# Kernel tuning notes

Hardware: AMD Instinct MI355X
Metric: run time of the kernel (lower is better)

The kernel has to match this reference:

```python
import jax, jax.numpy as jnp
import numpy as np

NX, NY, NT = 128, 128, 64          # global space-time grid
LX, LY = 2.0, 2.0                  # periodic domain extents
K_NB = 128                         # neighbors per query
NHEAD = 4
EPS = 1e-5


def setup_inputs() -> dict:
    key = jax.random.key(0)
    ks = jax.random.split(key, 12)
    N = NX * NY * NT
    B, d, dff, L = 2048, 64, 128, 2
    nrm = lambda k, s: jax.random.normal(k, s, jnp.float32) * 0.05
    return {
        "q_lin_idx": jax.random.randint(ks[0], (B,), 0, N),
        "offsets_ijk": jax.random.randint(ks[1], (K_NB, 3), 0, 8),
        "coords": jax.random.uniform(ks[2], (N, 3), jnp.float32) * 2.0,
        "vals": jax.random.normal(ks[3], (N, 3), jnp.float32),
        "log_gammas": jnp.zeros((3,), jnp.float32),
        "proj_w": nrm(ks[4], (d, 6)), "proj_b": jnp.zeros((d,), jnp.float32),
        "qkv_w": nrm(ks[5], (L, 3 * d, d)), "qkv_b": jnp.zeros((L, 3 * d), jnp.float32),
        "out_w": nrm(ks[6], (L, d, d)), "out_b": jnp.zeros((L, d), jnp.float32),
        "ln1_s": jnp.ones((L, d), jnp.float32), "ln1_b": jnp.zeros((L, d), jnp.float32),
        "ff1_w": nrm(ks[7], (L, dff, d)), "ff1_b": jnp.zeros((L, dff), jnp.float32),
        "ff2_w": nrm(ks[8], (L, d, dff)), "ff2_b": jnp.zeros((L, d), jnp.float32),
        "ln2_s": jnp.ones((L, d), jnp.float32), "ln2_b": jnp.zeros((L, d), jnp.float32),
        "head_ln_s": jnp.ones((d,), jnp.float32), "head_ln_b": jnp.zeros((d,), jnp.float32),
        "head1_w": nrm(ks[9], (d, d)), "head1_b": jnp.zeros((d,), jnp.float32),
        "head2_w": nrm(ks[10], (3, d)), "head2_b": jnp.zeros((3,), jnp.float32),
    }


def _ln(x, s, b):
    m = x.mean(-1, keepdims=True)
    v = ((x - m) ** 2).mean(-1, keepdims=True)
    return (x - m) * jax.lax.rsqrt(v + EPS) * s + b


def _dper(a, b, L):
    # periodic relative delta in [-L/2, L/2)
    return (a - b + 0.5 * L) % L - 0.5 * L


def reference(q_lin_idx, offsets_ijk, coords, vals, log_gammas, proj_w, proj_b,
              qkv_w, qkv_b, out_w, out_b, ln1_s, ln1_b, ff1_w, ff1_b, ff2_w, ff2_b,
              ln2_s, ln2_b, head_ln_s, head_ln_b, head1_w, head1_b, head2_w, head2_b):
    # --- periodic-wrapped neighbor indices (div/mod on linear index) ---
    i = q_lin_idx // (NY * NT)
    r = q_lin_idx % (NY * NT)
    j = r // NT
    kk = r % NT
    di, dj, dk = offsets_ijk[:, 0], offsets_ijk[:, 1], offsets_ijk[:, 2]
    I = (i[:, None] + di[None, :]) % NX          # wrap_x
    J = (j[:, None] + dj[None, :]) % NY          # wrap_y
    T = jnp.clip(kk[:, None] + dk[None, :], 0, NT - 1)  # no wrap in t
    nb = I * (NY * NT) + J * NT + T              # [B, K]

    # --- gather + relative-delta encode ---
    q_xyz = coords[q_lin_idx]                    # [B, 3]
    nb_xyz = coords[nb]                          # [B, K, 3]
    dx = _dper(nb_xyz[..., 0], q_xyz[:, None, 0], LX)
    dy = _dper(nb_xyz[..., 1], q_xyz[:, None, 1], LY)
    dt = nb_xyz[..., 2] - q_xyz[:, None, 2]
    rel = jnp.stack([dx, dy, dt], -1) * jnp.exp(log_gammas)[None, None, :]
    tokens = jnp.concatenate([rel, vals[nb]], -1)  # [B, K, 6]

    # --- input projection + TransformerEncoder (post-norm, relu FF) ---
    h = tokens @ proj_w.T + proj_b               # [B, S, d]
    B, S, d = h.shape
    dh = d // NHEAD
    scale = 1.0 / np.sqrt(dh).astype(np.float32)
    for l in range(qkv_w.shape[0]):
        qkv = h @ qkv_w[l].T + qkv_b[l]
        qh, kh, vh = jnp.split(qkv, 3, axis=-1)
        qh = qh.reshape(B, S, NHEAD, dh).transpose(0, 2, 1, 3)
        kh = kh.reshape(B, S, NHEAD, dh).transpose(0, 2, 1, 3)
        vh = vh.reshape(B, S, NHEAD, dh).transpose(0, 2, 1, 3)
        att = jax.nn.softmax(jnp.einsum('bhqd,bhkd->bhqk', qh, kh) * scale, axis=-1)
        o = jnp.einsum('bhqk,bhkd->bhqd', att, vh).transpose(0, 2, 1, 3).reshape(B, S, d)
        h = _ln(h + (o @ out_w[l].T + out_b[l]), ln1_s[l], ln1_b[l])
        ff = jax.nn.relu(h @ ff1_w[l].T + ff1_b[l]) @ ff2_w[l].T + ff2_b[l]
        h = _ln(h + ff, ln2_s[l], ln2_b[l])

    # --- mean pool over neighbors + head ---
    hm = h.mean(axis=1)                          # [B, d]
    g = _ln(hm, head_ln_s, head_ln_b)
    g = jax.nn.gelu(g @ head1_w.T + head1_b, approximate=False)
    return g @ head2_w.T + head2_b               # [B, 3]
```

## Files before the change

### kernel.cpp

```cpp
#include <hip/hip_runtime.h>
#include <math.h>

#define NXg 128
#define NYg 128
#define NTg 64
#define SEQ 128
#define DIM 64
#define NH 4
#define DHd 16
#define DFFd 128
#define NLAYER 2
#define EPSf 1e-5f

typedef _Float16 f16x8 __attribute__((ext_vector_type(8)));
typedef _Float16 f16x4 __attribute__((ext_vector_type(4)));
typedef __fp16 fp16x2 __attribute__((ext_vector_type(2)));
typedef float f32x4 __attribute__((ext_vector_type(4)));

#define MFMA16(a, b, c) __builtin_amdgcn_mfma_f32_16x16x32_f16(a, b, c, 0, 0, 0)

union FragU { int d[4]; f16x8 v; };
union H4U  { int d[2]; f16x4 v; };
union P2U  { int i; fp16x2 h; };

__device__ __forceinline__ int pk2(float a, float b) {
  P2U u;
  u.h = __builtin_amdgcn_cvt_pkrtz(a, b);
  return u.i;
}
__device__ __forceinline__ float2 up2(int p) {
  P2U u; u.i = p;
  return make_float2((float)u.h[0], (float)u.h[1]);
}

__device__ __forceinline__ f16x8 zero8() {
  f16x8 z;
#pragma unroll
  for (int i = 0; i < 8; ++i) z[i] = (_Float16)0.0f;
  return z;
}
__device__ __forceinline__ f32x4 zero4f() {
  f32x4 z;
  z[0] = 0.f; z[1] = 0.f; z[2] = 0.f; z[3] = 0.f;
  return z;
}
__device__ __forceinline__ f16x8 ld8(const _Float16* p) { return *(const f16x8*)p; }

__device__ __forceinline__ f16x8 frag_k16p(int p0, int p1, int quad, int l15) {
  int slA = ((2 * quad) * 16 + l15) & 63;
  int slB = ((2 * quad + 1) * 16 + l15) & 63;
  FragU u;
  u.d[0] = __shfl(p0, slA, 64);
  u.d[1] = __shfl(p1, slA, 64);
  u.d[2] = __shfl(p0, slB, 64);
  u.d[3] = __shfl(p1, slB, 64);
  if (quad >= 2) { u.d[0] = 0; u.d[1] = 0; u.d[2] = 0; u.d[3] = 0; }
  return u.v;
}

__device__ __forceinline__ f16x8 frag_k64(const int* pk, int kt, int quad, int l15) {
  const int slA = (2 * (quad & 1)) * 16 + l15;
  const int slB = (2 * (quad & 1) + 1) * 16 + l15;
  const bool hi = quad >= 2;
  int a0 = __shfl(pk[4 * kt + 0], slA, 64), b0 = __shfl(pk[4 * kt + 2], slA, 64);
  int a1 = __shfl(pk[4 * kt + 1], slA, 64), b1 = __shfl(pk[4 * kt + 3], slA, 64);
  int a2 = __shfl(pk[4 * kt + 0], slB, 64), b2 = __shfl(pk[4 * kt + 2], slB, 64);
  int a3 = __shfl(pk[4 * kt + 1], slB, 64), b3 = __shfl(pk[4 * kt + 3], slB, 64);
  FragU u;
  u.d[0] = hi ? b0 : a0;
  u.d[1] = hi ? b1 : a1;
  u.d[2] = hi ? b2 : a2;
  u.d[3] = hi ? b3 : a3;
  return u.v;
}

__device__ __forceinline__ void res_ln_qt(const f32x4 acc[4], int pkX[8],
                                          const float* __restrict__ bias,
                                          const float* __restrict__ lns,
                                          const float* __restrict__ lnb,
                                          int quad) {
  float v[4][4];
  float s = 0.f;
#pragma unroll
  for (int mt = 0; mt < 4; ++mt) {
    f32x4 bb = *(const f32x4*)(bias + mt * 16 + quad * 4);
    float2 x0 = up2(pkX[mt * 2 + 0]);
    float2 x1 = up2(pkX[mt * 2 + 1]);
    v[mt][0] = acc[mt][0] + bb[0] + x0.x;
    v[mt][1] = acc[mt][1] + bb[1] + x0.y;
    v[mt][2] = acc[mt][2] + bb[2] + x1.x;
    v[mt][3] = acc[mt][3] + bb[3] + x1.y;
    s += (v[mt][0] + v[mt][1]) + (v[mt][2] + v[mt][3]);
  }
  s += __shfl_xor(s, 16, 64);
  s += __shfl_xor(s, 32, 64);
  const float mu = s * (1.0f / 64.0f);
  float q2 = 0.f;
#pragma unroll
  for (int mt = 0; mt < 4; ++mt)
#pragma unroll
    for (int jr = 0; jr < 4; ++jr) { float d = v[mt][jr] - mu; q2 = fmaf(d, d, q2); }
  q2 += __shfl_xor(q2, 16, 64);
  q2 += __shfl_xor(q2, 32, 64);
  const float rstd = rsqrtf(q2 * (1.0f / 64.0f) + EPSf);
#pragma unroll
  for (int mt = 0; mt < 4; ++mt) {
    f32x4 sv = *(const f32x4*)(lns + mt * 16 + quad * 4);
    f32x4 bv = *(const f32x4*)(lnb + mt * 16 + quad * 4);
    float o0 = fmaf((v[mt][0] - mu) * rstd, sv[0], bv[0]);
    float o1 = fmaf((v[mt][1] - mu) * rstd, sv[1], bv[1]);
    float o2 = fmaf((v[mt][2] - mu) * rstd, sv[2], bv[2]);
    float o3 = fmaf((v[mt][3] - mu) * rstd, sv[3], bv[3]);
    pkX[mt * 2 + 0] = pk2(o0, o1);
    pkX[mt * 2 + 1] = pk2(o2, o3);
  }
}

__global__ void prep_weights(const float* __restrict__ qkv_w,
                             const float* __restrict__ out_w,
                             const float* __restrict__ ff1_w,
                             const float* __restrict__ ff2_w,
                             _Float16* __restrict__ wsH) {
  int i = blockIdx.x * 256 + threadIdx.x;
  if (i < 24576) wsH[i] = (_Float16)qkv_w[i];
  else if (i < 32768) wsH[i] = (_Float16)out_w[i - 24576];
  else if (i < 49152) wsH[i] = (_Float16)ff1_w[i - 32768];
  else if (i < 65536) wsH[i] = (_Float16)ff2_w[i - 49152];
}

__global__ __launch_bounds__(256, 2)
void fieldformer_mfma(const int* __restrict__ q_lin_idx,
                      const int* __restrict__ offsets_ijk,
                      const float* __restrict__ coords,
                      const float* __restrict__ vals,
                      const float* __restrict__ log_gammas,
                      const float* __restrict__ proj_w,
                      const float* __restrict__ proj_b,
                      const float* __restrict__ qkv_b,
                      const float* __restrict__ out_b,
                      const float* __restrict__ ln1_s,
                      const float* __restrict__ ln1_b,
                      const float* __restrict__ ff1_b,
                      const float* __restrict__ ff2_b,
                      const float* __restrict__ ln2_s,
                      const float* __restrict__ ln2_b,
                      const float* __restrict__ head_ln_s,
                      const float* __restrict__ head_ln_b,
                      const float* __restrict__ head1_w,
                      const float* __restrict__ head1_b,
                      const float* __restrict__ head2_w,
                      const float* __restrict__ head2_b,
                      const _Float16* __restrict__ wH,
                      float* __restrict__ out) {
  __shared__ __align__(16) _Float16 sK[128 * 72];
  __shared__ __align__(16) _Float16 sV[64 * 136];

  const int tid = threadIdx.x;
  const int wv = tid >> 6;
  const int lane = tid & 63;
  const int quad = lane >> 4;
  const int l15 = lane & 15;
  const int b = blockIdx.x;

  {
    const int row = tid >> 1, hf = tid & 1;
    const int q = q_lin_idx[b];
    const int qi = q / (NYg * NTg);
    const int qrem = q - qi * (NYg * NTg);
    const int qj = qrem / NTg;
    const int qk = qrem - qj * NTg;
    const int di = offsets_ijk[row * 3 + 0];
    const int dj = offsets_ijk[row * 3 + 1];
    const int dk = offsets_ijk[row * 3 + 2];
    const int I = (qi + di) % NXg;
    const int J = (qj + dj) % NYg;
    int T = qk + dk; T = T < 0 ? 0 : (T > NTg - 1 ? NTg - 1 : T);
    const int nb = I * (NYg * NTg) + J * NTg + T;
    const float qx = coords[q * 3 + 0], qy = coords[q * 3 + 1], qz = coords[q * 3 + 2];
    const float nx_ = coords[nb * 3 + 0], ny_ = coords[nb * 3 + 1], nz_ = coords[nb * 3 + 2];
    float ax = nx_ - qx + 1.0f; ax -= 2.0f * floorf(ax * 0.5f); ax -= 1.0f;
    float ay = ny_ - qy + 1.0f; ay -= 2.0f * floorf(ay * 0.5f); ay -= 1.0f;
    const float at = nz_ - qz;
    float tok[6];
    tok[0] = ax * expf(log_gammas[0]);
    tok[1] = ay * expf(log_gammas[1]);
    tok[2] = at * expf(log_gammas[2]);
    tok[3] = vals[nb * 3 + 0];
    tok[4] = vals[nb * 3 + 1];
    tok[5] = vals[nb * 3 + 2];
#pragma unroll
    for (int ci = 0; ci < 32; ++ci) {
      const int c = hf * 32 + ci;
      const float* w = proj_w + c * 6;
      float a = proj_b[c];
      a = fmaf(tok[0], w[0], a); a = fmaf(tok[1], w[1], a);
      a = fmaf(tok[2], w[2], a); a = fmaf(tok[3], w[3], a);
      a = fmaf(tok[4], w[4], a); a = fmaf(tok[5], w[5], a);
      sK[row * 72 + c] = (_Float16)a;
    }
  }
  __syncthreads();

  int pkX[2][8];
#pragma unroll
  for (int qt = 0; qt < 2; ++qt) {
    const int q = (wv * 2 + qt) * 16 + l15;
#pragma unroll
    for (int mt = 0; mt < 4; ++mt) {
      int2 t = *(const int2*)(sK + q * 72 + mt * 16 + quad * 4);
      pkX[qt][mt * 2 + 0] = t.x;
      pkX[qt][mt * 2 + 1] = t.y;
    }
  }

  for (int l = 0; l < NLAYER; ++l) {
    const _Float16* qkvH = wH + l * 192 * 64;
    const _Float16* woutH = wH + 24576 + l * 64 * 64;
    const _Float16* ff1H = wH + 32768 + l * 128 * 64;
    const _Float16* ff2H = wH + 49152 + l * 64 * 128;
    const float* bqkv = qkv_b + l * 192;

    __syncthreads();

    f16x8 bxf[2][2];
#pragma unroll
    for (int qt = 0; qt < 2; ++qt)
#pragma unroll
      for (int kt = 0; kt < 2; ++kt) bxf[qt][kt] = frag_k64(pkX[qt], kt, quad, l15);

    int pkQ[2][8];
#pragma unroll
    for (int hd = 0; hd < NH; ++hd) {
      f32x4 dq[2] = {zero4f(), zero4f()};
      f32x4 dk[2] = {zero4f(), zero4f()};
      f32x4 dv[2] = {zero4f(), zero4f()};
#pragma unroll
      for (int kt = 0; kt < 2; ++kt) {
        f16x8 awq = ld8(qkvH + (hd * 16 + l15) * 64 + kt * 32 + quad * 8);
        f16x8 awk = ld8(qkvH + (64 + hd * 16 + l15) * 64 + kt * 32 + quad * 8);
        f16x8 awv = ld8(qkvH + (128 + hd * 16 + l15) * 64 + kt * 32 + quad * 8);
#pragma unroll
        for (int qt = 0; qt < 2; ++qt) {
          dq[qt] = MFMA16(awq, bxf[qt][kt], dq[qt]);
          dk[qt] = MFMA16(awk, bxf[qt][kt], dk[qt]);
          dv[qt] = MFMA16(awv, bxf[qt][kt], dv[qt]);
        }
      }
      const f32x4 bq4 = *(const f32x4*)(bqkv + hd * 16 + quad * 4);
      const f32x4 bk4 = *(const f32x4*)(bqkv + 64 + hd * 16 + quad * 4);
      const f32x4 bv4 = *(const f32x4*)(bqkv + 128 + hd * 16 + quad * 4);
#pragma unroll
      for (int qt = 0; qt < 2; ++qt) {
        const int q = (wv * 2 + qt) * 16 + l15;
        H4U k4;
        k4.d[0] = pk2(dk[qt][0] + bk4[0], dk[qt][1] + bk4[1]);
        k4.d[1] = pk2(dk[qt][2] + bk4[2], dk[qt][3] + bk4[3]);
        *(f16x4*)(sK + q * 72 + hd * 16 + quad * 4) = k4.v;
#pragma unroll
        for (int jr = 0; jr < 4; ++jr)
          sV[(hd * 16 + quad * 4 + jr) * 136 + q] = (_Float16)(dv[qt][jr] + bv4[jr]);
        pkQ[qt][hd * 2 + 0] = pk2((dq[qt][0] + bq4[0]) * 0.25f, (dq[qt][1] + bq4[1]) * 0.25f);
        pkQ[qt][hd * 2 + 1] = pk2((dq[qt][2] + bq4[2]) * 0.25f, (dq[qt][3] + bq4[3]) * 0.25f);
      }
    }
    __syncthreads();

    int pkO[2][8];
#pragma unroll
    for (int hd = 0; hd < NH; ++hd) {
#pragma unroll
      for (int qt = 0; qt < 2; ++qt) {
        f16x8 bqf = frag_k16p(pkQ[qt][hd * 2 + 0], pkQ[qt][hd * 2 + 1], quad, l15);
        float s0 = 0.f;
        int pkP[16];
#pragma unroll
        for (int mt = 0; mt < 8; ++mt) {
          f16x8 ak = (quad < 2) ? ld8(sK + (mt * 16 + l15) * 72 + hd * 16 + quad * 8)
                                : zero8();
          f32x4 zc = zero4f();
          f32x4 sc = MFMA16(ak, bqf, zc);
          float e0 = __expf(sc[0]), e1 = __expf(sc[1]);
          float e2 = __expf(sc[2]), e3 = __expf(sc[3]);
          s0 += (e0 + e1) + (e2 + e3);
          pkP[mt * 2 + 0] = pk2(e0, e1);
          pkP[mt * 2 + 1] = pk2(e2, e3);
        }
        s0 += __shfl_xor(s0, 16, 64);
        s0 += __shfl_xor(s0, 32, 64);
        const float inv = 1.0f / s0;
        f32x4 ov = zero4f();
#pragma unroll
        for (int kt2 = 0; kt2 < 4; ++kt2) {
          f16x8 av = ld8(sV + (hd * 16 + l15) * 136 + kt2 * 32 + quad * 8);
          f16x8 bp = frag_k64(pkP + 8 * (kt2 >> 1), kt2 & 1, quad, l15);
          ov = MFMA16(av, bp, ov);
        }
        pkO[qt][hd * 2 + 0] = pk2(ov[0] * inv, ov[1] * inv);
        pkO[qt][hd * 2 + 1] = pk2(ov[2] * inv, ov[3] * inv);
      }
    }

#pragma unroll
    for (int qt = 0; qt < 2; ++qt) {
      f32x4 y2[4] = {zero4f(), zero4f(), zero4f(), zero4f()};
#pragma unroll
      for (int kt = 0; kt < 2; ++kt) {
        f16x8 bof = frag_k64(pkO[qt], kt, quad, l15);
#pragma unroll
        for (int mt = 0; mt < 4; ++mt) {
          f16x8 aw = ld8(woutH + (mt * 16 + l15) * 64 + kt * 32 + quad * 8);
          y2[mt] = MFMA16(aw, bof, y2[mt]);
        }
      }
      res_ln_qt(y2, pkX[qt], out_b + l * 64, ln1_s + l * 64, ln1_b + l * 64, quad);
    }

#pragma unroll
    for (int qt = 0; qt < 2; ++qt) {
      f16x8 bx2[2];
#pragma unroll
      for (int kt = 0; kt < 2; ++kt) bx2[kt] = frag_k64(pkX[qt], kt, quad, l15);
      const float* b1 = ff1_b + l * 128;
      int pkH[16];
#pragma unroll
      for (int mt = 0; mt < 8; ++mt) {
        f32x4 f8 = zero4f();
#pragma unroll
        for (int kt = 0; kt < 2; ++kt) {
          f16x8 aw = ld8(ff1H + (mt * 16 + l15) * 64 + kt * 32 + quad * 8);
          f8 = MFMA16(aw, bx2[kt], f8);
        }
        f32x4 bb = *(const f32x4*)(b1 + mt * 16 + quad * 4);
        pkH[mt * 2 + 0] = pk2(fmaxf(f8[0] + bb[0], 0.f), fmaxf(f8[1] + bb[1], 0.f));
        pkH[mt * 2 + 1] = pk2(fmaxf(f8[2] + bb[2], 0.f), fmaxf(f8[3] + bb[3], 0.f));
      }
      f32x4 g4[4] = {zero4f(), zero4f(), zero4f(), zero4f()};
#pragma unroll
      for (int kt = 0; kt < 4; ++kt) {
        f16x8 bh = frag_k64(pkH + 8 * (kt >> 1), kt & 1, quad, l15);
#pragma unroll
        for (int mt = 0; mt < 4; ++mt) {
          f16x8 aw = ld8(ff2H + (mt * 16 + l15) * 128 + kt * 32 + quad * 8);
          g4[mt] = MFMA16(aw, bh, g4[mt]);
        }
      }
      res_ln_qt(g4, pkX[qt], ff2_b + l * 64, ln2_s + l * 64, ln2_b + l * 64, quad);
    }
  }

  __syncthreads();
  {
    float* pf = (float*)sK;
    float* gsc = pf + 256;
    float* asc = gsc + 64;
    f32x4 cs[4];
#pragma unroll
    for (int mt = 0; mt < 4; ++mt) {
      float2 a0 = up2(pkX[0][mt * 2 + 0]), a1 = up2(pkX[0][mt * 2 + 1]);
      float2 b0 = up2(pkX[1][mt * 2 + 0]), b1 = up2(pkX[1][mt * 2 + 1]);
      cs[mt][0] = a0.x + b0.x;
      cs[mt][1] = a0.y + b0.y;
      cs[mt][2] = a1.x + b1.x;
      cs[mt][3] = a1.y + b1.y;
    }
#pragma unroll
    for (int d = 1; d <= 8; d <<= 1)
#pragma unroll
      for (int mt = 0; mt < 4; ++mt)
#pragma unroll
        for (int jr = 0; jr < 4; ++jr) cs[mt][jr] += __shfl_xor(cs[mt][jr], d, 64);
    if (l15 == 0) {
#pragma unroll
      for (int mt = 0; mt < 4; ++mt)
        *(f32x4*)(pf + wv * 64 + mt * 16 + quad * 4) = cs[mt];
    }
    __syncthreads();
    if (tid < 64) {
      const float hm = (pf[tid] + pf[64 + tid] + pf[128 + tid] + pf[192 + tid]) * (1.0f / 128.0f);
      float t = hm;
      t += __shfl_xor(t, 1, 64);  t += __shfl_xor(t, 2, 64);
      t += __shfl_xor(t, 4, 64);  t += __shfl_xor(t, 8, 64);
      t += __shfl_xor(t, 16, 64); t += __shfl_xor(t, 32, 64);
      const float mu = t * (1.0f / 64.0f);
      const float dv = hm - mu;
      float v2 = dv * dv;
      v2 += __shfl_xor(v2, 1, 64);  v2 += __shfl_xor(v2, 2, 64);
      v2 += __shfl_xor(v2, 4, 64);  v2 += __shfl_xor(v2, 8, 64);
      v2 += __shfl_xor(v2, 16, 64); v2 += __shfl_xor(v2, 32, 64);
      const float var = v2 * (1.0f / 64.0f);
      gsc[tid] = fmaf(dv * rsqrtf(var + EPSf), head_ln_s[tid], head_ln_b[tid]);
    }
    __syncthreads();
    if (tid < 64) {
      float z = head1_b[tid];
      for (int k = 0; k < 64; ++k) z = fmaf(gsc[k], head1_w[tid * 64 + k], z);
      asc[tid] = 0.5f * z * (1.0f + erff(z * 0.70710678118654752f));
    }
    __syncthreads();
    if (tid < 3) {
      float z = head2_b[tid];
      for (int k = 0; k < 64; ++k) z = fmaf(asc[k], head2_w[tid * 64 + k], z);
      out[b * 3 + tid] = z;
    }
  }
}

extern "C" void kernel_launch(void* const* d_in, const int* in_sizes, int n_in,
                              void* d_out, int out_size, void* d_ws, size_t ws_size,
                              hipStream_t stream) {
  (void)n_in; (void)ws_size; (void)out_size;
  const int B = in_sizes[0];
  _Float16* wsH = (_Float16*)d_ws;

  prep_weights<<<dim3(256), dim3(256), 0, stream>>>(
      (const float*)d_in[7],
      (const float*)d_in[9],
      (const float*)d_in[13],
      (const float*)d_in[15],
      wsH);

  fieldformer_mfma<<<dim3(B), dim3(256), 0, stream>>>(
      (const int*)d_in[0],
      (const int*)d_in[1],
      (const float*)d_in[2],
      (const float*)d_in[3],
      (const float*)d_in[4],
      (const float*)d_in[5],
      (const float*)d_in[6],
      (const float*)d_in[8],
      (const float*)d_in[10],
      (const float*)d_in[11],
      (const float*)d_in[12],
      (const float*)d_in[14],
      (const float*)d_in[16],
      (const float*)d_in[17],
      (const float*)d_in[18],
      (const float*)d_in[19],
      (const float*)d_in[20],
      (const float*)d_in[21],
      (const float*)d_in[22],
      (const float*)d_in[23],
      (const float*)d_in[24],
      wsH,
      (float*)d_out);
}
```

Baseline: 342.7 us.

## Stream attention probs and FFN hidden chunks to cut registers, raise occupancy

Raises the launch-bounds occupancy hint from 2 to 3 blocks per CU. To fit the tighter register budget, the attention loop now computes each 32-key chunk of exp-scores and feeds it straight into the PV MFMA, so the full 16-int probability array is no longer held. The FFN does the same, producing ff1 hidden chunks just before their ff2 MFMAs, and the QKV input fragments are scoped so they die earlier. The risks are spills if the compiler cannot meet the new register cap, and less independent MFMA work in flight per wave.

```diff
diff --git a/kernel.cpp b/kernel.cpp
--- a/kernel.cpp
+++ b/kernel.cpp
@@ -128,7 +128,7 @@
   else if (i < 65536) wsH[i] = (_Float16)ff2_w[i - 49152];
 }
 
-__global__ __launch_bounds__(256, 2)
+__global__ __launch_bounds__(256, 3)
 void fieldformer_mfma(const int* __restrict__ q_lin_idx,
                       const int* __restrict__ offsets_ijk,
                       const float* __restrict__ coords,
@@ -222,45 +222,46 @@
 
     __syncthreads();
 
-    f16x8 bxf[2][2];
-#pragma unroll
-    for (int qt = 0; qt < 2; ++qt)
-#pragma unroll
-      for (int kt = 0; kt < 2; ++kt) bxf[qt][kt] = frag_k64(pkX[qt], kt, quad, l15);
-
     int pkQ[2][8];
-#pragma unroll
-    for (int hd = 0; hd < NH; ++hd) {
-      f32x4 dq[2] = {zero4f(), zero4f()};
-      f32x4 dk[2] = {zero4f(), zero4f()};
-      f32x4 dv[2] = {zero4f(), zero4f()};
-#pragma unroll
-      for (int kt = 0; kt < 2; ++kt) {
-        f16x8 awq = ld8(qkvH + (hd * 16 + l15) * 64 + kt * 32 + quad * 8);
-        f16x8 awk = ld8(qkvH + (64 + hd * 16 + l15) * 64 + kt * 32 + quad * 8);
-        f16x8 awv = ld8(qkvH + (128 + hd * 16 + l15) * 64 + kt * 32 + quad * 8);
+    {
+      f16x8 bxf[2][2];
+#pragma unroll
+      for (int qt = 0; qt < 2; ++qt)
+#pragma unroll
+        for (int kt = 0; kt < 2; ++kt) bxf[qt][kt] = frag_k64(pkX[qt], kt, quad, l15);
+#pragma unroll
+      for (int hd = 0; hd < NH; ++hd) {
+        f32x4 dq[2] = {zero4f(), zero4f()};
+        f32x4 dk[2] = {zero4f(), zero4f()};
+        f32x4 dv[2] = {zero4f(), zero4f()};
+#pragma unroll
+        for (int kt = 0; kt < 2; ++kt) {
+          f16x8 awq = ld8(qkvH + (hd * 16 + l15) * 64 + kt * 32 + quad * 8);
+          f16x8 awk = ld8(qkvH + (64 + hd * 16 + l15) * 64 + kt * 32 + quad * 8);
+          f16x8 awv = ld8(qkvH + (128 + hd * 16 + l15) * 64 + kt * 32 + quad * 8);
+#pragma unroll
+          for (int qt = 0; qt < 2; ++qt) {
+            dq[qt] = MFMA16(awq, bxf[qt][kt], dq[qt]);
+            dk[qt] = MFMA16(awk, bxf[qt][kt], dk[qt]);
+            dv[qt] = MFMA16(awv, bxf[qt][kt], dv[qt]);
+          }
+        }
+        const f32x4 bq4 = *(const f32x4*)(bqkv + hd * 16 + quad * 4);
+        const f32x4 bk4 = *(const f32x4*)(bqkv + 64 + hd * 16 + quad * 4);
+        const f32x4 bv4 = *(const f32x4*)(bqkv + 128 + hd * 16 + quad * 4);
 #pragma unroll
         for (int qt = 0; qt < 2; ++qt) {
-          dq[qt] = MFMA16(awq, bxf[qt][kt], dq[qt]);
-          dk[qt] = MFMA16(awk, bxf[qt][kt], dk[qt]);
-          dv[qt] = MFMA16(awv, bxf[qt][kt], dv[qt]);
-        }
-      }
-      const f32x4 bq4 = *(const f32x4*)(bqkv + hd * 16 + quad * 4);
-      const f32x4 bk4 = *(const f32x4*)(bqkv + 64 + hd * 16 + quad * 4);
-      const f32x4 bv4 = *(const f32x4*)(bqkv + 128 + hd * 16 + quad * 4);
-#pragma unroll
-      for (int qt = 0; qt < 2; ++qt) {
-        const int q = (wv * 2 + qt) * 16 + l15;
-        H4U k4;
-        k4.d[0] = pk2(dk[qt][0] + bk4[0], dk[qt][1] + bk4[1]);
-        k4.d[1] = pk2(dk[qt][2] + bk4[2], dk[qt][3] + bk4[3]);
-        *(f16x4*)(sK + q * 72 + hd * 16 + quad * 4) = k4.v;
-#pragma unroll
-        for (int jr = 0; jr < 4; ++jr)
-          sV[(hd * 16 + quad * 4 + jr) * 136 + q] = (_Float16)(dv[qt][jr] + bv4[jr]);
-        pkQ[qt][hd * 2 + 0] = pk2((dq[qt][0] + bq4[0]) * 0.25f, (dq[qt][1] + bq4[1]) * 0.25f);
-        pkQ[qt][hd * 2 + 1] = pk2((dq[qt][2] + bq4[2]) * 0.25f, (dq[qt][3] + bq4[3]) * 0.25f);
+          const int q = (wv * 2 + qt) * 16 + l15;
+          H4U k4;
+          k4.d[0] = pk2(dk[qt][0] + bk4[0], dk[qt][1] + bk4[1]);
+          k4.d[1] = pk2(dk[qt][2] + bk4[2], dk[qt][3] + bk4[3]);
+          *(f16x4*)(sK + q * 72 + hd * 16 + quad * 4) = k4.v;
+#pragma unroll
+          for (int jr = 0; jr < 4; ++jr)
+            sV[(hd * 16 + quad * 4 + jr) * 136 + q] = (_Float16)(dv[qt][jr] + bv4[jr]);
+          pkQ[qt][hd * 2 + 0] = pk2((dq[qt][0] + bq4[0]) * 0.25f, (dq[qt][1] + bq4[1]) * 0.25f);
+          pkQ[qt][hd * 2 + 1] = pk2((dq[qt][2] + bq4[2]) * 0.25f, (dq[qt][3] + bq4[3]) * 0.25f);
+        }
       }
     }
     __syncthreads();
@@ -272,29 +273,30 @@
       for (int qt = 0; qt < 2; ++qt) {
         f16x8 bqf = frag_k16p(pkQ[qt][hd * 2 + 0], pkQ[qt][hd * 2 + 1], quad, l15);
         float s0 = 0.f;
-        int pkP[16];
-#pragma unroll
-        for (int mt = 0; mt < 8; ++mt) {
-          f16x8 ak = (quad < 2) ? ld8(sK + (mt * 16 + l15) * 72 + hd * 16 + quad * 8)
-                                : zero8();
-          f32x4 zc = zero4f();
-          f32x4 sc = MFMA16(ak, bqf, zc);
-          float e0 = __expf(sc[0]), e1 = __expf(sc[1]);
-          float e2 = __expf(sc[2]), e3 = __expf(sc[3]);
-          s0 += (e0 + e1) + (e2 + e3);
-          pkP[mt * 2 + 0] = pk2(e0, e1);
-          pkP[mt * 2 + 1] = pk2(e2, e3);
+        f32x4 ov = zero4f();
+#pragma unroll
+        for (int kt2 = 0; kt2 < 4; ++kt2) {
+          int pkP[4];
+#pragma unroll
+          for (int mi = 0; mi < 2; ++mi) {
+            const int mt = kt2 * 2 + mi;
+            f16x8 ak = (quad < 2) ? ld8(sK + (mt * 16 + l15) * 72 + hd * 16 + quad * 8)
+                                  : zero8();
+            f32x4 zc = zero4f();
+            f32x4 sc = MFMA16(ak, bqf, zc);
+            float e0 = __expf(sc[0]), e1 = __expf(sc[1]);
+            float e2 = __expf(sc[2]), e3 = __expf(sc[3]);
+            s0 += (e0 + e1) + (e2 + e3);
+            pkP[mi * 2 + 0] = pk2(e0, e1);
+            pkP[mi * 2 + 1] = pk2(e2, e3);
+          }
+          f16x8 av = ld8(sV + (hd * 16 + l15) * 136 + kt2 * 32 + quad * 8);
+          f16x8 bp = frag_k64(pkP, 0, quad, l15);
+          ov = MFMA16(av, bp, ov);
         }
         s0 += __shfl_xor(s0, 16, 64);
         s0 += __shfl_xor(s0, 32, 64);
         const float inv = 1.0f / s0;
-        f32x4 ov = zero4f();
-#pragma unroll
-        for (int kt2 = 0; kt2 < 4; ++kt2) {
-          f16x8 av = ld8(sV + (hd * 16 + l15) * 136 + kt2 * 32 + quad * 8);
-          f16x8 bp = frag_k64(pkP + 8 * (kt2 >> 1), kt2 & 1, quad, l15);
-          ov = MFMA16(av, bp, ov);
-        }
         pkO[qt][hd * 2 + 0] = pk2(ov[0] * inv, ov[1] * inv);
         pkO[qt][hd * 2 + 1] = pk2(ov[2] * inv, ov[3] * inv);
       }
@@ -321,27 +323,28 @@
 #pragma unroll
       for (int kt = 0; kt < 2; ++kt) bx2[kt] = frag_k64(pkX[qt], kt, quad, l15);
       const float* b1 = ff1_b + l * 128;
-      int pkH[16];
-#pragma unroll
-      for (int mt = 0; mt < 8; ++mt) {
-        f32x4 f8 = zero4f();
-#pragma unroll
-        for (int kt = 0; kt < 2; ++kt) {
-          f16x8 aw = ld8(ff1H + (mt * 16 + l15) * 64 + kt * 32 + quad * 8);
-          f8 = MFMA16(aw, bx2[kt], f8);
-        }
-        f32x4 bb = *(const f32x4*)(b1 + mt * 16 + quad * 4);
-        pkH[mt * 2 + 0] = pk2(fmaxf(f8[0] + bb[0], 0.f), fmaxf(f8[1] + bb[1], 0.f));
-        pkH[mt * 2 + 1] = pk2(fmaxf(f8[2] + bb[2], 0.f), fmaxf(f8[3] + bb[3], 0.f));
-      }
       f32x4 g4[4] = {zero4f(), zero4f(), zero4f(), zero4f()};
 #pragma unroll
       for (int kt = 0; kt < 4; ++kt) {
-        f16x8 bh = frag_k64(pkH + 8 * (kt >> 1), kt & 1, quad, l15);
-#pragma unroll
-        for (int mt = 0; mt < 4; ++mt) {
-          f16x8 aw = ld8(ff2H + (mt * 16 + l15) * 128 + kt * 32 + quad * 8);
-          g4[mt] = MFMA16(aw, bh, g4[mt]);
+        int pkH[4];
+#pragma unroll
+        for (int mi = 0; mi < 2; ++mi) {
+          const int mt = kt * 2 + mi;
+          f32x4 f8 = zero4f();
+#pragma unroll
+          for (int k2 = 0; k2 < 2; ++k2) {
+            f16x8 aw = ld8(ff1H + (mt * 16 + l15) * 64 + k2 * 32 + quad * 8);
+            f8 = MFMA16(aw, bx2[k2], f8);
+          }
+          f32x4 bb = *(const f32x4*)(b1 + mt * 16 + quad * 4);
+          pkH[mi * 2 + 0] = pk2(fmaxf(f8[0] + bb[0], 0.f), fmaxf(f8[1] + bb[1], 0.f));
+          pkH[mi * 2 + 1] = pk2(fmaxf(f8[2] + bb[2], 0.f), fmaxf(f8[3] + bb[3], 0.f));
+        }
+        f16x8 bh = frag_k64(pkH, 0, quad, l15);
+#pragma unroll
+        for (int mt2 = 0; mt2 < 4; ++mt2) {
+          f16x8 aw = ld8(ff2H + (mt2 * 16 + l15) * 128 + kt * 32 + quad * 8);
+          g4[mt2] = MFMA16(aw, bh, g4[mt2]);
         }
       }
       res_ln_qt(g4, pkX[qt], ff2_b + l * 64, ln2_s + l * 64, ln2_b + l * 64, quad);
```

Result: faster. 319.7 us (-6.7%).
